# Kernel tuning notes

Measured on AMD Instinct MI355X. Metric: run time of the kernel, lower is better.

The kernel has to match this reference:

```python
import jax, jax.numpy as jnp
import numpy as np

# NF4 codebook (bitsandbytes nf4 data type, 16 levels)
NF4_TABLE = np.array([
    -1.0, -0.6961928009986877, -0.5250730514526367, -0.39491748809814453,
    -0.28444138169288635, -0.18477343022823334, -0.09105003625154495, 0.0,
    0.07958029955625534, 0.16093020141124725, 0.24611230194568634,
    0.33791524171829224, 0.44070982933044434, 0.5626170039176941,
    0.7229568362236023, 1.0], dtype=np.float32)

BLOCKSIZE = 64
SCALING = 32.0 / 16.0  # lora_alpha / r


def setup_inputs() -> dict:
    key = jax.random.key(0)
    k1, k2, k3, k4, k5 = jax.random.split(key, 5)
    tokens, in_f, out_f, r = 256, 4096, 11008, 16
    x = jax.random.normal(k1, (tokens, in_f), dtype=jnp.float32)
    q_codes = jax.random.randint(k2, (out_f, in_f), 0, 16, dtype=jnp.int32)
    absmax = jax.random.uniform(k3, (out_f, in_f // BLOCKSIZE), dtype=jnp.float32)
    lora_A = jax.random.normal(k4, (r, in_f), dtype=jnp.float32) * (1.0 / np.sqrt(in_f))
    lora_B = jax.random.normal(k5, (out_f, r), dtype=jnp.float32) * 0.02
    return {"x": x, "q_codes": q_codes, "absmax": absmax,
            "lora_A": lora_A, "lora_B": lora_B}


def reference(x, q_codes, absmax, lora_A, lora_B):
    out_f, in_f = q_codes.shape
    nf4 = jnp.asarray(NF4_TABLE, dtype=x.dtype)
    # Dequantize: codebook lookup, then per-block absmax scale.
    W = nf4[q_codes].reshape(out_f, in_f // BLOCKSIZE, BLOCKSIZE)
    W = (W * absmax[:, :, None]).reshape(out_f, in_f)  # [out_f, in_f]
    # Base 4-bit linear (no bias in bnb Linear4bit default here).
    base = x @ W.T  # [tokens, out_f]
    # LoRA path: dropout p=0 is identity in eval; scaling = alpha/r.
    lora = (x @ lora_A.T) @ lora_B.T  # [tokens, r] -> [tokens, out_f]
    return base + lora * jnp.asarray(SCALING, dtype=x.dtype)
```

## Files before the change

### kernel.cpp

```cpp
#include <hip/hip_runtime.h>

typedef unsigned int uint;
typedef unsigned short ushort;

typedef __attribute__((ext_vector_type(8))) short bf16x8;
typedef __attribute__((ext_vector_type(4))) float f32x4;

#define TOK 256
#define OUTF 11008
#define INF 4096
#define BM 256
#define BN 32
#define BK 64
#define NKT 64
#define NTILES 344

__device__ __constant__ float NF4_TBL[16] = {
    -1.0f, -0.6961928009986877f, -0.5250730514526367f, -0.39491748809814453f,
    -0.28444138169288635f, -0.18477343022823334f, -0.09105003625154495f, 0.0f,
    0.07958029955625534f, 0.16093020141124725f, 0.24611230194568634f,
    0.33791524171829224f, 0.44070982933044434f, 0.5626170039176941f,
    0.7229568362236023f, 1.0f};

__device__ __forceinline__ ushort f2bf(float f) {
  return (ushort)((__float_as_uint(f) + 0x8000u) >> 16);
}

__device__ __forceinline__ void async_cp16(const void* g, void* l) {
  __builtin_amdgcn_global_load_lds(
      (const __attribute__((address_space(1))) uint*)g,
      (__attribute__((address_space(3))) uint*)l, 16, 0, 0);
}

__device__ __forceinline__ uint dq2(int ca, int cb, float amax, int tbits) {
  float fa = __int_as_float(__builtin_amdgcn_ds_bpermute(ca << 2, tbits)) * amax;
  float fb = __int_as_float(__builtin_amdgcn_ds_bpermute(cb << 2, tbits)) * amax;
  uint ua = (__float_as_uint(fa) + 0x8000u) >> 16;
  uint ub = (__float_as_uint(fb) + 0x8000u) & 0xffff0000u;
  return ua | ub;
}

__global__ void prep_kernel(const float4* __restrict__ x4, const float4* __restrict__ lB4,
                            ushort4* __restrict__ xbf4, ushort4* __restrict__ lBbf4) {
  const int stride = gridDim.x * blockDim.x;
  for (int idx = blockIdx.x * blockDim.x + threadIdx.x; idx < TOK * INF / 4; idx += stride) {
    float4 v = x4[idx];
    ushort4 o;
    o.x = f2bf(v.x); o.y = f2bf(v.y); o.z = f2bf(v.z); o.w = f2bf(v.w);
    xbf4[idx] = o;
  }
  for (int idx = blockIdx.x * blockDim.x + threadIdx.x; idx < OUTF * 16; idx += stride) {
    int n = idx >> 4, jq = idx & 15;
    ushort4 o = {0, 0, 0, 0};
    if (jq < 4) {
      float4 v = lB4[n * 4 + jq];
      o.x = f2bf(v.x); o.y = f2bf(v.y); o.z = f2bf(v.z); o.w = f2bf(v.w);
    }
    lBbf4[idx] = o;
  }
}

__global__ __launch_bounds__(1024)
void xa_kernel(const float* __restrict__ x, const float* __restrict__ lA,
               ushort* __restrict__ xa2) {
  const int m = blockIdx.x;
  const int t = threadIdx.x;
  const float4* x4 = (const float4*)(x + (size_t)m * INF);
  const float4* lA4 = (const float4*)lA;
  float4 xv = x4[t];
  float acc[16];
#pragma unroll
  for (int j = 0; j < 16; ++j) {
    float4 a = lA4[j * (INF / 4) + t];
    acc[j] = xv.x * a.x + xv.y * a.y + xv.z * a.z + xv.w * a.w;
  }
#pragma unroll
  for (int j = 0; j < 16; ++j)
#pragma unroll
    for (int s = 32; s > 0; s >>= 1) acc[j] += __shfl_xor(acc[j], s, 64);
  __shared__ float red[16][16];
  const int w = t >> 6, l = t & 63;
  if (l == 0) {
#pragma unroll
    for (int j = 0; j < 16; ++j) red[w][j] = acc[j];
  }
  __syncthreads();
  if (t < 64) {
    ushort v = 0;
    if (t < 16) {
      float s = 0.f;
#pragma unroll
      for (int w2 = 0; w2 < 16; ++w2) s += red[w2][t];
      v = f2bf(2.0f * s);
    }
    xa2[m * 64 + t] = v;
  }
}

__global__ __launch_bounds__(256, 4)
void gemm_kernel(const int* __restrict__ qc, const float* __restrict__ am,
                 const ushort* __restrict__ xbf, const ushort* __restrict__ lBbf,
                 const ushort* __restrict__ xa2, float* __restrict__ dest,
                 int kt_per) {
  __shared__ ushort Abuf[BM * BK];
  __shared__ ushort Bbuf[BN * BK];

  const int tid = threadIdx.x;
  const int w = tid >> 6;
  const int l = tid & 63;
  const int split = blockIdx.x / NTILES;
  const int ntile = blockIdx.x - split * NTILES;
  const int n0 = ntile * BN;
  const int k0t = split * kt_per;
  const int ktEnd = k0t + kt_per;

  const int tbits = __float_as_int(NF4_TBL[l & 15]);

  const int arow = w * 8 + (l >> 3);
  const int acol = ((l & 7) ^ (l >> 3)) << 3;

  const int brow = tid >> 3;
  const int bq = tid & 7;

  int aoff[2][4], boff[2][2];
#pragma unroll
  for (int ks = 0; ks < 2; ++ks) {
    const int cc = ks * 4 + (l >> 4);
#pragma unroll
    for (int mt = 0; mt < 4; ++mt) {
      int row = w * 64 + mt * 16 + (l & 15);
      aoff[ks][mt] = row * 64 + ((cc ^ (l & 7)) << 3);
    }
#pragma unroll
    for (int nt = 0; nt < 2; ++nt) {
      int row = nt * 16 + (l & 15);
      boff[ks][nt] = row * 64 + ((cc ^ (l & 7)) << 3);
    }
  }

  f32x4 acc[4][2];
#pragma unroll
  for (int mt = 0; mt < 4; ++mt)
#pragma unroll
    for (int nt = 0; nt < 2; ++nt) acc[mt][nt] = (f32x4){0.f, 0.f, 0.f, 0.f};

  const int* qbase = qc + (size_t)(n0 + brow) * INF + bq * 8;
  const float* ambase = am + (size_t)(n0 + brow) * 64;
  int4 c0 = ((const int4*)(qbase + (size_t)k0t * BK))[0];
  int4 c1 = ((const int4*)(qbase + (size_t)k0t * BK))[1];
  float amax = ambase[k0t];

  for (int kt = k0t; kt < ktEnd; ++kt) {
#pragma unroll
    for (int i = 0; i < 8; ++i) {
      const ushort* g = xbf + (size_t)(i * 32 + arow) * INF + kt * BK + acol;
      async_cp16(g, &Abuf[(i * 256 + w * 64) * 8]);
    }
    uint4 d;
    d.x = dq2(c0.x, c0.y, amax, tbits);
    d.y = dq2(c0.z, c0.w, amax, tbits);
    d.z = dq2(c1.x, c1.y, amax, tbits);
    d.w = dq2(c1.z, c1.w, amax, tbits);
    *(uint4*)&Bbuf[(brow * 8 + (bq ^ (brow & 7))) * 8] = d;
    if (kt + 1 < ktEnd) {
      c0 = ((const int4*)(qbase + (size_t)(kt + 1) * BK))[0];
      c1 = ((const int4*)(qbase + (size_t)(kt + 1) * BK))[1];
      amax = ambase[kt + 1];
    }
    __syncthreads();
#pragma unroll
    for (int ks = 0; ks < 2; ++ks) {
      bf16x8 a[4], b[2];
#pragma unroll
      for (int mt = 0; mt < 4; ++mt) a[mt] = *(const bf16x8*)&Abuf[aoff[ks][mt]];
#pragma unroll
      for (int nt = 0; nt < 2; ++nt) b[nt] = *(const bf16x8*)&Bbuf[boff[ks][nt]];
#pragma unroll
      for (int mt = 0; mt < 4; ++mt)
#pragma unroll
        for (int nt = 0; nt < 2; ++nt)
          acc[mt][nt] = __builtin_amdgcn_mfma_f32_16x16x32_bf16(a[mt], b[nt], acc[mt][nt], 0, 0, 0);
    }
    __syncthreads();
  }

  if (split == 0) {
#pragma unroll
    for (int i = 0; i < 8; ++i) {
      const ushort* g = xa2 + (i * 32 + arow) * 64 + acol;
      async_cp16(g, &Abuf[(i * 256 + w * 64) * 8]);
    }
    const ushort* g = lBbf + (size_t)(n0 + arow) * 64 + acol;
    async_cp16(g, &Bbuf[(w * 64) * 8]);
    __syncthreads();
#pragma unroll
    for (int ks = 0; ks < 2; ++ks) {
      bf16x8 a[4], b[2];
#pragma unroll
      for (int mt = 0; mt < 4; ++mt) a[mt] = *(const bf16x8*)&Abuf[aoff[ks][mt]];
#pragma unroll
      for (int nt = 0; nt < 2; ++nt) b[nt] = *(const bf16x8*)&Bbuf[boff[ks][nt]];
#pragma unroll
      for (int mt = 0; mt < 4; ++mt)
#pragma unroll
        for (int nt = 0; nt < 2; ++nt)
          acc[mt][nt] = __builtin_amdgcn_mfma_f32_16x16x32_bf16(a[mt], b[nt], acc[mt][nt], 0, 0, 0);
    }
    __syncthreads();
  }

  float* dst = dest + (size_t)split * TOK * OUTF;
#pragma unroll
  for (int mt = 0; mt < 4; ++mt) {
#pragma unroll
    for (int nt = 0; nt < 2; ++nt) {
      int col = n0 + nt * 16 + (l & 15);
#pragma unroll
      for (int r = 0; r < 4; ++r) {
        int row = w * 64 + mt * 16 + (l >> 4) * 4 + r;
        dst[(size_t)row * OUTF + col] = acc[mt][nt][r];
      }
    }
  }
}

__global__ void reduce_kernel(const float4* __restrict__ part, float4* __restrict__ out,
                              int ks) {
  const int QN = TOK * OUTF / 4;
  int i = blockIdx.x * blockDim.x + threadIdx.x;
  if (i < QN) {
    float4 s = part[i];
    for (int s2 = 1; s2 < ks; ++s2) {
      float4 p = part[(size_t)s2 * QN + i];
      s.x += p.x; s.y += p.y; s.z += p.z; s.w += p.w;
    }
    out[i] = s;
  }
}

extern "C" void kernel_launch(void* const* d_in, const int* in_sizes, int n_in,
                              void* d_out, int out_size, void* d_ws, size_t ws_size,
                              hipStream_t stream) {
  const float* x = (const float*)d_in[0];
  const int* qc = (const int*)d_in[1];
  const float* am = (const float*)d_in[2];
  const float* lA = (const float*)d_in[3];
  const float* lB = (const float*)d_in[4];
  float* out = (float*)d_out;

  const size_t off_lB = (size_t)TOK * INF * 2;
  const size_t off_xa2 = off_lB + (size_t)OUTF * 64 * 2;
  const size_t off_part = off_xa2 + (size_t)TOK * 64 * 2;
  const size_t part_bytes = (size_t)TOK * OUTF * 4;

  ushort* xbf = (ushort*)d_ws;
  ushort* lBbf = (ushort*)((char*)d_ws + off_lB);
  ushort* xa2 = (ushort*)((char*)d_ws + off_xa2);
  float* part = (float*)((char*)d_ws + off_part);

  int ks = 1;
  if (ws_size >= off_part + 4 * part_bytes) ks = 4;
  else if (ws_size >= off_part + 2 * part_bytes) ks = 2;
  float* dest = (ks == 1) ? out : part;

  prep_kernel<<<1024, 256, 0, stream>>>((const float4*)x, (const float4*)lB,
                                        (ushort4*)xbf, (ushort4*)lBbf);
  xa_kernel<<<TOK, 1024, 0, stream>>>(x, lA, xa2);
  gemm_kernel<<<NTILES * ks, 256, 0, stream>>>(qc, am, xbf, lBbf, xa2, dest, NKT / ks);
  if (ks > 1)
    reduce_kernel<<<(TOK * OUTF / 4 + 255) / 256, 256, 0, stream>>>((const float4*)part,
                                                                    (float4*)out, ks);
}
```

Before: 318.2 us.

## Drop LDS staging in GEMM; load MFMA operands directly into registers

```diff
diff --git a/kernel.cpp b/kernel.cpp
--- a/kernel.cpp
+++ b/kernel.cpp
@@ -9,10 +9,7 @@
 #define TOK 256
 #define OUTF 11008
 #define INF 4096
-#define BM 256
 #define BN 32
-#define BK 64
-#define NKT 64
 #define NTILES 344
 
 __device__ __constant__ float NF4_TBL[16] = {
@@ -26,18 +23,21 @@
   return (ushort)((__float_as_uint(f) + 0x8000u) >> 16);
 }
 
-__device__ __forceinline__ void async_cp16(const void* g, void* l) {
-  __builtin_amdgcn_global_load_lds(
-      (const __attribute__((address_space(1))) uint*)g,
-      (__attribute__((address_space(3))) uint*)l, 16, 0, 0);
-}
-
 __device__ __forceinline__ uint dq2(int ca, int cb, float amax, int tbits) {
   float fa = __int_as_float(__builtin_amdgcn_ds_bpermute(ca << 2, tbits)) * amax;
   float fb = __int_as_float(__builtin_amdgcn_ds_bpermute(cb << 2, tbits)) * amax;
   uint ua = (__float_as_uint(fa) + 0x8000u) >> 16;
   uint ub = (__float_as_uint(fb) + 0x8000u) & 0xffff0000u;
   return ua | ub;
+}
+
+__device__ __forceinline__ bf16x8 dq8(int4 c0, int4 c1, float amax, int tbits) {
+  union { uint4 u; bf16x8 b; } cv;
+  cv.u.x = dq2(c0.x, c0.y, amax, tbits);
+  cv.u.y = dq2(c0.z, c0.w, amax, tbits);
+  cv.u.z = dq2(c1.x, c1.y, amax, tbits);
+  cv.u.w = dq2(c1.z, c1.w, amax, tbits);
+  return cv.b;
 }
 
 __global__ void prep_kernel(const float4* __restrict__ x4, const float4* __restrict__ lB4,
@@ -97,128 +97,117 @@
   }
 }
 
-__global__ __launch_bounds__(256, 4)
+__global__ __launch_bounds__(256, 3)
 void gemm_kernel(const int* __restrict__ qc, const float* __restrict__ am,
                  const ushort* __restrict__ xbf, const ushort* __restrict__ lBbf,
                  const ushort* __restrict__ xa2, float* __restrict__ dest,
-                 int kt_per) {
-  __shared__ ushort Abuf[BM * BK];
-  __shared__ ushort Bbuf[BN * BK];
-
+                 int nst) {
   const int tid = threadIdx.x;
   const int w = tid >> 6;
   const int l = tid & 63;
+  const int chunk = l >> 4;
+  const int rlo = l & 15;
   const int split = blockIdx.x / NTILES;
   const int ntile = blockIdx.x - split * NTILES;
   const int n0 = ntile * BN;
-  const int k0t = split * kt_per;
-  const int ktEnd = k0t + kt_per;
-
-  const int tbits = __float_as_int(NF4_TBL[l & 15]);
-
-  const int arow = w * 8 + (l >> 3);
-  const int acol = ((l & 7) ^ (l >> 3)) << 3;
-
-  const int brow = tid >> 3;
-  const int bq = tid & 7;
-
-  int aoff[2][4], boff[2][2];
-#pragma unroll
-  for (int ks = 0; ks < 2; ++ks) {
-    const int cc = ks * 4 + (l >> 4);
-#pragma unroll
-    for (int mt = 0; mt < 4; ++mt) {
-      int row = w * 64 + mt * 16 + (l & 15);
-      aoff[ks][mt] = row * 64 + ((cc ^ (l & 7)) << 3);
-    }
+  const int k0 = split * nst * 32;
+
+  const int tbits = __float_as_int(NF4_TBL[rlo]);
+
+  const ushort* aptr[4];
+#pragma unroll
+  for (int mt = 0; mt < 4; ++mt)
+    aptr[mt] = xbf + (size_t)(w * 64 + mt * 16 + rlo) * INF + chunk * 8;
+  int col[2];
+  const int* qptr[2];
+  const float* amptr[2];
+#pragma unroll
+  for (int nt = 0; nt < 2; ++nt) {
+    col[nt] = n0 + nt * 16 + rlo;
+    qptr[nt] = qc + (size_t)col[nt] * INF + chunk * 8;
+    amptr[nt] = am + (size_t)col[nt] * 64;
+  }
+
+  f32x4 acc[4][2];
+#pragma unroll
+  for (int mt = 0; mt < 4; ++mt)
+#pragma unroll
+    for (int nt = 0; nt < 2; ++nt) acc[mt][nt] = (f32x4){0.f, 0.f, 0.f, 0.f};
+
+  bf16x8 a_c[4];
+  int4 c0_c[2], c1_c[2];
+  float ax_c[2];
+#pragma unroll
+  for (int mt = 0; mt < 4; ++mt) a_c[mt] = *(const bf16x8*)(aptr[mt] + k0);
+#pragma unroll
+  for (int nt = 0; nt < 2; ++nt) {
+    const int4* qp = (const int4*)(qptr[nt] + k0);
+    c0_c[nt] = qp[0];
+    c1_c[nt] = qp[1];
+    ax_c[nt] = amptr[nt][k0 >> 6];
+  }
+
+#pragma unroll 2
+  for (int s = 0; s < nst; ++s) {
+    const int k = k0 + s * 32;
+    bf16x8 a_n[4];
+    int4 c0_n[2], c1_n[2];
+    float ax_n[2];
+    if (s + 1 < nst) {
+      const int kn = k + 32;
+#pragma unroll
+      for (int mt = 0; mt < 4; ++mt) a_n[mt] = *(const bf16x8*)(aptr[mt] + kn);
+#pragma unroll
+      for (int nt = 0; nt < 2; ++nt) {
+        const int4* qp = (const int4*)(qptr[nt] + kn);
+        c0_n[nt] = qp[0];
+        c1_n[nt] = qp[1];
+        ax_n[nt] = amptr[nt][kn >> 6];
+      }
+    }
+    bf16x8 b[2];
+#pragma unroll
+    for (int nt = 0; nt < 2; ++nt) b[nt] = dq8(c0_c[nt], c1_c[nt], ax_c[nt], tbits);
+#pragma unroll
+    for (int mt = 0; mt < 4; ++mt)
+#pragma unroll
+      for (int nt = 0; nt < 2; ++nt)
+        acc[mt][nt] = __builtin_amdgcn_mfma_f32_16x16x32_bf16(a_c[mt], b[nt], acc[mt][nt], 0, 0, 0);
+    if (s + 1 < nst) {
+#pragma unroll
+      for (int mt = 0; mt < 4; ++mt) a_c[mt] = a_n[mt];
+#pragma unroll
+      for (int nt = 0; nt < 2; ++nt) {
+        c0_c[nt] = c0_n[nt]; c1_c[nt] = c1_n[nt]; ax_c[nt] = ax_n[nt];
+      }
+    }
+  }
+
+  if (split == 0) {
+    bf16x8 a_l[4], b_l[2];
+#pragma unroll
+    for (int mt = 0; mt < 4; ++mt)
+      a_l[mt] = *(const bf16x8*)(xa2 + (size_t)(w * 64 + mt * 16 + rlo) * 64 + chunk * 8);
+#pragma unroll
+    for (int nt = 0; nt < 2; ++nt)
+      b_l[nt] = *(const bf16x8*)(lBbf + (size_t)col[nt] * 64 + chunk * 8);
+#pragma unroll
+    for (int mt = 0; mt < 4; ++mt)
+#pragma unroll
+      for (int nt = 0; nt < 2; ++nt)
+        acc[mt][nt] = __builtin_amdgcn_mfma_f32_16x16x32_bf16(a_l[mt], b_l[nt], acc[mt][nt], 0, 0, 0);
+  }
+
+  float* dst = dest + (size_t)split * TOK * OUTF;
+#pragma unroll
+  for (int mt = 0; mt < 4; ++mt) {
 #pragma unroll
     for (int nt = 0; nt < 2; ++nt) {
-      int row = nt * 16 + (l & 15);
-      boff[ks][nt] = row * 64 + ((cc ^ (l & 7)) << 3);
-    }
-  }
-
-  f32x4 acc[4][2];
-#pragma unroll
-  for (int mt = 0; mt < 4; ++mt)
-#pragma unroll
-    for (int nt = 0; nt < 2; ++nt) acc[mt][nt] = (f32x4){0.f, 0.f, 0.f, 0.f};
-
-  const int* qbase = qc + (size_t)(n0 + brow) * INF + bq * 8;
-  const float* ambase = am + (size_t)(n0 + brow) * 64;
-  int4 c0 = ((const int4*)(qbase + (size_t)k0t * BK))[0];
-  int4 c1 = ((const int4*)(qbase + (size_t)k0t * BK))[1];
-  float amax = ambase[k0t];
-
-  for (int kt = k0t; kt < ktEnd; ++kt) {
-#pragma unroll
-    for (int i = 0; i < 8; ++i) {
-      const ushort* g = xbf + (size_t)(i * 32 + arow) * INF + kt * BK + acol;
-      async_cp16(g, &Abuf[(i * 256 + w * 64) * 8]);
-    }
-    uint4 d;
-    d.x = dq2(c0.x, c0.y, amax, tbits);
-    d.y = dq2(c0.z, c0.w, amax, tbits);
-    d.z = dq2(c1.x, c1.y, amax, tbits);
-    d.w = dq2(c1.z, c1.w, amax, tbits);
-    *(uint4*)&Bbuf[(brow * 8 + (bq ^ (brow & 7))) * 8] = d;
-    if (kt + 1 < ktEnd) {
-      c0 = ((const int4*)(qbase + (size_t)(kt + 1) * BK))[0];
-      c1 = ((const int4*)(qbase + (size_t)(kt + 1) * BK))[1];
-      amax = ambase[kt + 1];
-    }
-    __syncthreads();
-#pragma unroll
-    for (int ks = 0; ks < 2; ++ks) {
-      bf16x8 a[4], b[2];
-#pragma unroll
-      for (int mt = 0; mt < 4; ++mt) a[mt] = *(const bf16x8*)&Abuf[aoff[ks][mt]];
-#pragma unroll
-      for (int nt = 0; nt < 2; ++nt) b[nt] = *(const bf16x8*)&Bbuf[boff[ks][nt]];
-#pragma unroll
-      for (int mt = 0; mt < 4; ++mt)
-#pragma unroll
-        for (int nt = 0; nt < 2; ++nt)
-          acc[mt][nt] = __builtin_amdgcn_mfma_f32_16x16x32_bf16(a[mt], b[nt], acc[mt][nt], 0, 0, 0);
-    }
-    __syncthreads();
-  }
-
-  if (split == 0) {
-#pragma unroll
-    for (int i = 0; i < 8; ++i) {
-      const ushort* g = xa2 + (i * 32 + arow) * 64 + acol;
-      async_cp16(g, &Abuf[(i * 256 + w * 64) * 8]);
-    }
-    const ushort* g = lBbf + (size_t)(n0 + arow) * 64 + acol;
-    async_cp16(g, &Bbuf[(w * 64) * 8]);
-    __syncthreads();
-#pragma unroll
-    for (int ks = 0; ks < 2; ++ks) {
-      bf16x8 a[4], b[2];
-#pragma unroll
-      for (int mt = 0; mt < 4; ++mt) a[mt] = *(const bf16x8*)&Abuf[aoff[ks][mt]];
-#pragma unroll
-      for (int nt = 0; nt < 2; ++nt) b[nt] = *(const bf16x8*)&Bbuf[boff[ks][nt]];
-#pragma unroll
-      for (int mt = 0; mt < 4; ++mt)
-#pragma unroll
-        for (int nt = 0; nt < 2; ++nt)
-          acc[mt][nt] = __builtin_amdgcn_mfma_f32_16x16x32_bf16(a[mt], b[nt], acc[mt][nt], 0, 0, 0);
-    }
-    __syncthreads();
-  }
-
-  float* dst = dest + (size_t)split * TOK * OUTF;
-#pragma unroll
-  for (int mt = 0; mt < 4; ++mt) {
-#pragma unroll
-    for (int nt = 0; nt < 2; ++nt) {
-      int col = n0 + nt * 16 + (l & 15);
+      int c = n0 + nt * 16 + rlo;
 #pragma unroll
       for (int r = 0; r < 4; ++r) {
         int row = w * 64 + mt * 16 + (l >> 4) * 4 + r;
-        dst[(size_t)row * OUTF + col] = acc[mt][nt][r];
+        dst[(size_t)row * OUTF + c] = acc[mt][nt][r];
       }
     }
   }
@@ -263,10 +252,10 @@
   else if (ws_size >= off_part + 2 * part_bytes) ks = 2;
   float* dest = (ks == 1) ? out : part;
 
-  prep_kernel<<<1024, 256, 0, stream>>>((const float4*)x, (const float4*)lB,
+  prep_kernel<<<2048, 256, 0, stream>>>((const float4*)x, (const float4*)lB,
                                         (ushort4*)xbf, (ushort4*)lBbf);
   xa_kernel<<<TOK, 1024, 0, stream>>>(x, lA, xa2);
-  gemm_kernel<<<NTILES * ks, 256, 0, stream>>>(qc, am, xbf, lBbf, xa2, dest, NKT / ks);
+  gemm_kernel<<<NTILES * ks, 256, 0, stream>>>(qc, am, xbf, lBbf, xa2, dest, 128 / ks);
   if (ks > 1)
     reduce_kernel<<<(TOK * OUTF / 4 + 255) / 256, 256, 0, stream>>>((const float4*)part,
                                                                     (float4*)out, ks);
```

After: 457.1 us. 1.44x slower.

## Pre-pack NF4 codes to nibbles, switch to fp16 MFMA with wider N tiles

Applied to the files above, without the earlier changes.

```diff
diff --git a/kernel.cpp b/kernel.cpp
--- a/kernel.cpp
+++ b/kernel.cpp
@@ -1,19 +1,18 @@
 #include <hip/hip_runtime.h>
+#include <hip/hip_fp16.h>
 
 typedef unsigned int uint;
 typedef unsigned short ushort;
 
-typedef __attribute__((ext_vector_type(8))) short bf16x8;
+typedef __attribute__((ext_vector_type(8))) _Float16 f16x8;
 typedef __attribute__((ext_vector_type(4))) float f32x4;
 
 #define TOK 256
 #define OUTF 11008
 #define INF 4096
 #define BM 256
-#define BN 32
-#define BK 64
-#define NKT 64
-#define NTILES 344
+#define BN 64
+#define NT2 172
 
 __device__ __constant__ float NF4_TBL[16] = {
     -1.0f, -0.6961928009986877f, -0.5250730514526367f, -0.39491748809814453f,
@@ -22,8 +21,8 @@
     0.33791524171829224f, 0.44070982933044434f, 0.5626170039176941f,
     0.7229568362236023f, 1.0f};
 
-__device__ __forceinline__ ushort f2bf(float f) {
-  return (ushort)((__float_as_uint(f) + 0x8000u) >> 16);
+__device__ __forceinline__ ushort f2h(float f) {
+  return __half_as_ushort(__float2half(f));
 }
 
 __device__ __forceinline__ void async_cp16(const void* g, void* l) {
@@ -32,31 +31,32 @@
       (__attribute__((address_space(3))) uint*)l, 16, 0, 0);
 }
 
-__device__ __forceinline__ uint dq2(int ca, int cb, float amax, int tbits) {
-  float fa = __int_as_float(__builtin_amdgcn_ds_bpermute(ca << 2, tbits)) * amax;
-  float fb = __int_as_float(__builtin_amdgcn_ds_bpermute(cb << 2, tbits)) * amax;
-  uint ua = (__float_as_uint(fa) + 0x8000u) >> 16;
-  uint ub = (__float_as_uint(fb) + 0x8000u) & 0xffff0000u;
-  return ua | ub;
-}
-
-__global__ void prep_kernel(const float4* __restrict__ x4, const float4* __restrict__ lB4,
-                            ushort4* __restrict__ xbf4, ushort4* __restrict__ lBbf4) {
+__global__ void prep_kernel(const int4* __restrict__ qc4, uint* __restrict__ pk,
+                            const float4* __restrict__ x4, ushort4* __restrict__ xh4,
+                            const float4* __restrict__ lB4, ushort4* __restrict__ lBh4) {
   const int stride = gridDim.x * blockDim.x;
-  for (int idx = blockIdx.x * blockDim.x + threadIdx.x; idx < TOK * INF / 4; idx += stride) {
-    float4 v = x4[idx];
+  const int t0 = blockIdx.x * blockDim.x + threadIdx.x;
+  for (int d = t0; d < OUTF * INF / 8; d += stride) {
+    int4 a = qc4[2 * d];
+    int4 b = qc4[2 * d + 1];
+    pk[d] = (uint)(a.x & 15) | ((uint)(a.y & 15) << 4) | ((uint)(a.z & 15) << 8) |
+            ((uint)(a.w & 15) << 12) | ((uint)(b.x & 15) << 16) | ((uint)(b.y & 15) << 20) |
+            ((uint)(b.z & 15) << 24) | ((uint)(b.w & 15) << 28);
+  }
+  for (int i = t0; i < TOK * INF / 4; i += stride) {
+    float4 v = x4[i];
     ushort4 o;
-    o.x = f2bf(v.x); o.y = f2bf(v.y); o.z = f2bf(v.z); o.w = f2bf(v.w);
-    xbf4[idx] = o;
-  }
-  for (int idx = blockIdx.x * blockDim.x + threadIdx.x; idx < OUTF * 16; idx += stride) {
-    int n = idx >> 4, jq = idx & 15;
+    o.x = f2h(v.x); o.y = f2h(v.y); o.z = f2h(v.z); o.w = f2h(v.w);
+    xh4[i] = o;
+  }
+  for (int i = t0; i < OUTF * 16; i += stride) {
+    int n = i >> 4, jq = i & 15;
     ushort4 o = {0, 0, 0, 0};
     if (jq < 4) {
       float4 v = lB4[n * 4 + jq];
-      o.x = f2bf(v.x); o.y = f2bf(v.y); o.z = f2bf(v.z); o.w = f2bf(v.w);
-    }
-    lBbf4[idx] = o;
+      o.x = f2h(v.x); o.y = f2h(v.y); o.z = f2h(v.z); o.w = f2h(v.w);
+    }
+    lBh4[i] = o;
   }
 }
 
@@ -91,134 +91,126 @@
       float s = 0.f;
 #pragma unroll
       for (int w2 = 0; w2 < 16; ++w2) s += red[w2][t];
-      v = f2bf(2.0f * s);
+      v = f2h(2.0f * s);
     }
     xa2[m * 64 + t] = v;
   }
 }
 
-__global__ __launch_bounds__(256, 4)
-void gemm_kernel(const int* __restrict__ qc, const float* __restrict__ am,
-                 const ushort* __restrict__ xbf, const ushort* __restrict__ lBbf,
-                 const ushort* __restrict__ xa2, float* __restrict__ dest,
-                 int kt_per) {
-  __shared__ ushort Abuf[BM * BK];
-  __shared__ ushort Bbuf[BN * BK];
+__global__ __launch_bounds__(256, 3)
+void gemm_kernel(const uint* __restrict__ pk, const float* __restrict__ am,
+                 const ushort* __restrict__ xh, const ushort* __restrict__ lBh,
+                 const ushort* __restrict__ xa2, float* __restrict__ dest, int nst) {
+  __shared__ ushort Abuf[BM * 64];
+  __shared__ __half2 tbl[256];
 
   const int tid = threadIdx.x;
   const int w = tid >> 6;
   const int l = tid & 63;
-  const int split = blockIdx.x / NTILES;
-  const int ntile = blockIdx.x - split * NTILES;
+  const int chunk = l >> 4;
+  const int rlo = l & 15;
+  const int split = blockIdx.x / NT2;
+  const int ntile = blockIdx.x - split * NT2;
   const int n0 = ntile * BN;
-  const int k0t = split * kt_per;
-  const int ktEnd = k0t + kt_per;
-
-  const int tbits = __float_as_int(NF4_TBL[l & 15]);
+  const int k0 = split * nst * 64;
+
+  tbl[tid & 255] = __halves2half2(__float2half(NF4_TBL[tid & 15]),
+                                  __float2half(NF4_TBL[(tid >> 4) & 15]));
 
   const int arow = w * 8 + (l >> 3);
   const int acol = ((l & 7) ^ (l >> 3)) << 3;
 
-  const int brow = tid >> 3;
-  const int bq = tid & 7;
-
-  int aoff[2][4], boff[2][2];
+  int aoff[2][4];
 #pragma unroll
   for (int ks = 0; ks < 2; ++ks) {
-    const int cc = ks * 4 + (l >> 4);
-#pragma unroll
-    for (int mt = 0; mt < 4; ++mt) {
-      int row = w * 64 + mt * 16 + (l & 15);
-      aoff[ks][mt] = row * 64 + ((cc ^ (l & 7)) << 3);
-    }
-#pragma unroll
-    for (int nt = 0; nt < 2; ++nt) {
-      int row = nt * 16 + (l & 15);
-      boff[ks][nt] = row * 64 + ((cc ^ (l & 7)) << 3);
-    }
-  }
-
-  f32x4 acc[4][2];
+    const int cc = ks * 4 + chunk;
+#pragma unroll
+    for (int mt = 0; mt < 4; ++mt)
+      aoff[ks][mt] = (w * 64 + mt * 16 + rlo) * 64 + ((cc ^ (l & 7)) << 3);
+  }
+
+  int col[4];
+  const char* qp[4];
+  const float* amp[4];
+#pragma unroll
+  for (int nt = 0; nt < 4; ++nt) {
+    col[nt] = n0 + nt * 16 + rlo;
+    qp[nt] = (const char*)pk + (size_t)col[nt] * (INF / 2) + (k0 >> 1) + chunk * 4;
+    amp[nt] = am + (size_t)col[nt] * 64 + (k0 >> 6);
+  }
+
+  f32x4 acc[4][4];
 #pragma unroll
   for (int mt = 0; mt < 4; ++mt)
 #pragma unroll
-    for (int nt = 0; nt < 2; ++nt) acc[mt][nt] = (f32x4){0.f, 0.f, 0.f, 0.f};
-
-  const int* qbase = qc + (size_t)(n0 + brow) * INF + bq * 8;
-  const float* ambase = am + (size_t)(n0 + brow) * 64;
-  int4 c0 = ((const int4*)(qbase + (size_t)k0t * BK))[0];
-  int4 c1 = ((const int4*)(qbase + (size_t)k0t * BK))[1];
-  float amax = ambase[k0t];
-
-  for (int kt = k0t; kt < ktEnd; ++kt) {
+    for (int nt = 0; nt < 4; ++nt) acc[mt][nt] = (f32x4){0.f, 0.f, 0.f, 0.f};
+
+  for (int s = 0; s < nst; ++s) {
+    const int kb = k0 + s * 64;
 #pragma unroll
     for (int i = 0; i < 8; ++i) {
-      const ushort* g = xbf + (size_t)(i * 32 + arow) * INF + kt * BK + acol;
+      const ushort* g = xh + (size_t)(i * 32 + arow) * INF + kb + acol;
       async_cp16(g, &Abuf[(i * 256 + w * 64) * 8]);
     }
-    uint4 d;
-    d.x = dq2(c0.x, c0.y, amax, tbits);
-    d.y = dq2(c0.z, c0.w, amax, tbits);
-    d.z = dq2(c1.x, c1.y, amax, tbits);
-    d.w = dq2(c1.z, c1.w, amax, tbits);
-    *(uint4*)&Bbuf[(brow * 8 + (bq ^ (brow & 7))) * 8] = d;
-    if (kt + 1 < ktEnd) {
-      c0 = ((const int4*)(qbase + (size_t)(kt + 1) * BK))[0];
-      c1 = ((const int4*)(qbase + (size_t)(kt + 1) * BK))[1];
-      amax = ambase[kt + 1];
+    uint qd[4][2];
+    __half2 ax2[4];
+#pragma unroll
+    for (int nt = 0; nt < 4; ++nt) {
+      qd[nt][0] = *(const uint*)(qp[nt] + s * 32);
+      qd[nt][1] = *(const uint*)(qp[nt] + s * 32 + 16);
+      ax2[nt] = __float2half2_rn(amp[nt][s]);
     }
     __syncthreads();
 #pragma unroll
     for (int ks = 0; ks < 2; ++ks) {
-      bf16x8 a[4], b[2];
-#pragma unroll
-      for (int mt = 0; mt < 4; ++mt) a[mt] = *(const bf16x8*)&Abuf[aoff[ks][mt]];
-#pragma unroll
-      for (int nt = 0; nt < 2; ++nt) b[nt] = *(const bf16x8*)&Bbuf[boff[ks][nt]];
+      f16x8 a[4];
+#pragma unroll
+      for (int mt = 0; mt < 4; ++mt) a[mt] = *(const f16x8*)&Abuf[aoff[ks][mt]];
+      f16x8 b[4];
+#pragma unroll
+      for (int nt = 0; nt < 4; ++nt) {
+        uint dw = qd[nt][ks];
+        union { __half2 h[4]; f16x8 v; } u;
+        u.h[0] = __hmul2(tbl[dw & 255], ax2[nt]);
+        u.h[1] = __hmul2(tbl[(dw >> 8) & 255], ax2[nt]);
+        u.h[2] = __hmul2(tbl[(dw >> 16) & 255], ax2[nt]);
+        u.h[3] = __hmul2(tbl[dw >> 24], ax2[nt]);
+        b[nt] = u.v;
+      }
 #pragma unroll
       for (int mt = 0; mt < 4; ++mt)
 #pragma unroll
-        for (int nt = 0; nt < 2; ++nt)
-          acc[mt][nt] = __builtin_amdgcn_mfma_f32_16x16x32_bf16(a[mt], b[nt], acc[mt][nt], 0, 0, 0);
+        for (int nt = 0; nt < 4; ++nt)
+          acc[mt][nt] = __builtin_amdgcn_mfma_f32_16x16x32_f16(a[mt], b[nt], acc[mt][nt], 0, 0, 0);
     }
     __syncthreads();
   }
 
   if (split == 0) {
-#pragma unroll
-    for (int i = 0; i < 8; ++i) {
-      const ushort* g = xa2 + (i * 32 + arow) * 64 + acol;
-      async_cp16(g, &Abuf[(i * 256 + w * 64) * 8]);
-    }
-    const ushort* g = lBbf + (size_t)(n0 + arow) * 64 + acol;
-    async_cp16(g, &Bbuf[(w * 64) * 8]);
-    __syncthreads();
-#pragma unroll
-    for (int ks = 0; ks < 2; ++ks) {
-      bf16x8 a[4], b[2];
-#pragma unroll
-      for (int mt = 0; mt < 4; ++mt) a[mt] = *(const bf16x8*)&Abuf[aoff[ks][mt]];
-#pragma unroll
-      for (int nt = 0; nt < 2; ++nt) b[nt] = *(const bf16x8*)&Bbuf[boff[ks][nt]];
-#pragma unroll
-      for (int mt = 0; mt < 4; ++mt)
-#pragma unroll
-        for (int nt = 0; nt < 2; ++nt)
-          acc[mt][nt] = __builtin_amdgcn_mfma_f32_16x16x32_bf16(a[mt], b[nt], acc[mt][nt], 0, 0, 0);
-    }
-    __syncthreads();
+    f16x8 a_l[4], b_l[4];
+#pragma unroll
+    for (int mt = 0; mt < 4; ++mt)
+      a_l[mt] = *(const f16x8*)(xa2 + (size_t)(w * 64 + mt * 16 + rlo) * 64 + chunk * 8);
+#pragma unroll
+    for (int nt = 0; nt < 4; ++nt)
+      b_l[nt] = *(const f16x8*)(lBh + (size_t)col[nt] * 64 + chunk * 8);
+#pragma unroll
+    for (int mt = 0; mt < 4; ++mt)
+#pragma unroll
+      for (int nt = 0; nt < 4; ++nt)
+        acc[mt][nt] = __builtin_amdgcn_mfma_f32_16x16x32_f16(a_l[mt], b_l[nt], acc[mt][nt], 0, 0, 0);
   }
 
   float* dst = dest + (size_t)split * TOK * OUTF;
 #pragma unroll
   for (int mt = 0; mt < 4; ++mt) {
 #pragma unroll
-    for (int nt = 0; nt < 2; ++nt) {
-      int col = n0 + nt * 16 + (l & 15);
+    for (int nt = 0; nt < 4; ++nt) {
+      int c = col[nt];
 #pragma unroll
       for (int r = 0; r < 4; ++r) {
-        int row = w * 64 + mt * 16 + (l >> 4) * 4 + r;
-        dst[(size_t)row * OUTF + col] = acc[mt][nt][r];
+        int row = w * 64 + mt * 16 + chunk * 4 + r;
+        dst[(size_t)row * OUTF + c] = acc[mt][nt][r];
       }
     }
   }
@@ -250,12 +242,14 @@
 
   const size_t off_lB = (size_t)TOK * INF * 2;
   const size_t off_xa2 = off_lB + (size_t)OUTF * 64 * 2;
-  const size_t off_part = off_xa2 + (size_t)TOK * 64 * 2;
+  const size_t off_pk = off_xa2 + (size_t)TOK * 64 * 2;
+  const size_t off_part = off_pk + (size_t)OUTF * INF / 2;
   const size_t part_bytes = (size_t)TOK * OUTF * 4;
 
-  ushort* xbf = (ushort*)d_ws;
-  ushort* lBbf = (ushort*)((char*)d_ws + off_lB);
+  ushort* xh = (ushort*)d_ws;
+  ushort* lBh = (ushort*)((char*)d_ws + off_lB);
   ushort* xa2 = (ushort*)((char*)d_ws + off_xa2);
+  uint* pk = (uint*)((char*)d_ws + off_pk);
   float* part = (float*)((char*)d_ws + off_part);
 
   int ks = 1;
@@ -263,10 +257,10 @@
   else if (ws_size >= off_part + 2 * part_bytes) ks = 2;
   float* dest = (ks == 1) ? out : part;
 
-  prep_kernel<<<1024, 256, 0, stream>>>((const float4*)x, (const float4*)lB,
-                                        (ushort4*)xbf, (ushort4*)lBbf);
+  prep_kernel<<<4096, 256, 0, stream>>>((const int4*)qc, pk, (const float4*)x,
+                                        (ushort4*)xh, (const float4*)lB, (ushort4*)lBh);
   xa_kernel<<<TOK, 1024, 0, stream>>>(x, lA, xa2);
-  gemm_kernel<<<NTILES * ks, 256, 0, stream>>>(qc, am, xbf, lBbf, xa2, dest, NKT / ks);
+  gemm_kernel<<<NT2 * ks, 256, 0, stream>>>(pk, am, xh, lBh, xa2, dest, 64 / ks);
   if (ks > 1)
     reduce_kernel<<<(TOK * OUTF / 4 + 255) / 256, 256, 0, stream>>>((const float4*)part,
                                                                     (float4*)out, ks);
```

Result: slower. 371.2 us (+16.7%).
